# Performance work log

Hardware: AMD Instinct MI355X
Metric: run time of the kernel (lower is better)

Reference implementation:

```python
import jax, jax.numpy as jnp
import numpy as np
from jax import lax

FEAT_STRIDE = 16
RATIOS = (0.5, 1.0, 2.0)
SCALES = (8.0, 16.0, 32.0)
N_ANCHOR = len(RATIOS) * len(SCALES)  # 9
PRE_NMS = 6000     # ProposalCreator test-mode n_pre_nms
POST_NMS = 300     # test-mode n_post_nms
NMS_THRESH = 0.7
MIN_SIZE = 16.0


def _anchor_base():
    base = 16.0
    py = px = base / 2.0
    r = np.asarray(RATIOS, np.float64)
    s = np.asarray(SCALES, np.float64)
    h = (base * s[None, :] * np.sqrt(r[:, None])).reshape(-1)
    w = (base * s[None, :] * np.sqrt(1.0 / r[:, None])).reshape(-1)
    return np.stack([py - h / 2, px - w / 2, py + h / 2, px + w / 2], axis=1).astype(np.float32)  # [9,4] (y1,x1,y2,x2)


def _enumerate_anchors(H, W):
    base = _anchor_base()
    sy = np.arange(H, dtype=np.float32) * FEAT_STRIDE
    sx = np.arange(W, dtype=np.float32) * FEAT_STRIDE
    yy, xx = np.meshgrid(sy, sx, indexing='ij')
    shift = np.stack([yy, xx, yy, xx], axis=-1).reshape(-1, 1, 4)  # [H*W,1,4]
    return jnp.asarray((shift + base[None]).reshape(-1, 4))  # [H*W*9, 4]


def _loc2bbox(anchors, loc):
    h = anchors[:, 2] - anchors[:, 0]
    w = anchors[:, 3] - anchors[:, 1]
    cy = anchors[:, 0] + 0.5 * h
    cx = anchors[:, 1] + 0.5 * w
    dy, dx, dh, dw = loc[:, 0], loc[:, 1], loc[:, 2], loc[:, 3]
    ny, nx = dy * h + cy, dx * w + cx
    nh, nw = jnp.exp(dh) * h, jnp.exp(dw) * w
    return jnp.stack([ny - 0.5 * nh, nx - 0.5 * nw, ny + 0.5 * nh, nx + 0.5 * nw], axis=1)


def _iou_one(box, boxes):
    ty1 = jnp.maximum(box[0], boxes[:, 0])
    tx1 = jnp.maximum(box[1], boxes[:, 1])
    ty2 = jnp.minimum(box[2], boxes[:, 2])
    tx2 = jnp.minimum(box[3], boxes[:, 3])
    inter = jnp.clip(ty2 - ty1, 0.0) * jnp.clip(tx2 - tx1, 0.0)
    a1 = (box[2] - box[0]) * (box[3] - box[1])
    a2 = (boxes[:, 2] - boxes[:, 0]) * (boxes[:, 3] - boxes[:, 1])
    return inter / jnp.maximum(a1 + a2 - inter, 1e-9)


def _nms_keep(boxes, valid):
    # boxes are sorted by descending score; greedy suppression, fixed shapes
    n = boxes.shape[0]
    idxs = jnp.arange(n)
    def body(i, keep):
        iou = _iou_one(boxes[i], boxes)
        sup = (iou > NMS_THRESH) & (idxs > i)
        return jnp.where(keep[i], keep & ~sup, keep)
    return lax.fori_loop(0, n, body, valid)


def _propose_one(loc, fg, anchors, img_h, img_w, scale):
    boxes = _loc2bbox(anchors, loc)
    boxes = jnp.stack([jnp.clip(boxes[:, 0], 0.0, img_h), jnp.clip(boxes[:, 1], 0.0, img_w),
                       jnp.clip(boxes[:, 2], 0.0, img_h), jnp.clip(boxes[:, 3], 0.0, img_w)], axis=1)
    min_sz = MIN_SIZE * scale
    hs = boxes[:, 2] - boxes[:, 0]
    ws = boxes[:, 3] - boxes[:, 1]
    ok = (hs >= min_sz) & (ws >= min_sz)
    sc = jnp.where(ok, fg, -jnp.inf)
    top_sc, top_idx = lax.top_k(sc, PRE_NMS)
    b = boxes[top_idx]
    keep = _nms_keep(b, jnp.isfinite(top_sc))
    # stable-compact kept boxes to the front, pad to POST_NMS with zeros
    order = jnp.argsort(jnp.where(keep, jnp.arange(PRE_NMS), PRE_NMS))
    sel = order[:POST_NMS]
    n_keep = jnp.sum(keep)
    mask = (jnp.arange(POST_NMS) < n_keep)[:, None].astype(b.dtype)
    return b[sel] * mask  # [POST_NMS, 4], zero-padded


def setup_inputs() -> dict:
    key = jax.random.key(0)
    ks = jax.random.split(key, 5)
    B, C, H, W = 16, 512, 50, 50
    x = jax.random.normal(ks[0], (B, C, H, W), jnp.float32)
    conv1_w = 0.01 * jax.random.normal(ks[1], (512, 512, 3, 3), jnp.float32)
    conv1_b = jnp.zeros((512,), jnp.float32)
    score_w = 0.01 * jax.random.normal(ks[2], (N_ANCHOR * 2, 512, 1, 1), jnp.float32)
    score_b = jnp.zeros((N_ANCHOR * 2,), jnp.float32)
    loc_w = 0.01 * jax.random.normal(ks[3], (N_ANCHOR * 4, 512, 1, 1), jnp.float32)
    loc_b = jnp.zeros((N_ANCHOR * 4,), jnp.float32)
    return {"x": x, "img_h": 800, "img_w": 800,
            "conv1_w": conv1_w, "conv1_b": conv1_b,
            "score_w": score_w, "score_b": score_b,
            "loc_w": loc_w, "loc_b": loc_b}


def reference(x, img_h, img_w, conv1_w, conv1_b, score_w, score_b, loc_w, loc_b):
    B, C, H, W = x.shape
    anchors = _enumerate_anchors(H, W)
    # Faithful to the source bug: `mid = self.conv1(x); mid = relu(x)` -> conv1 output is discarded.
    mid = jax.nn.relu(x)
    # 1x1 convs as einsum; permute(0,2,3,1) + view == bhwo layout then reshape
    locs = jnp.einsum('bchw,oc->bhwo', mid, loc_w[:, :, 0, 0]) + loc_b      # [B,H,W,4A]
    locs = locs.reshape(B, -1, 4)                                            # [B, H*W*A, 4]
    scores_raw = jnp.einsum('bchw,oc->bhwo', mid, score_w[:, :, 0, 0]) + score_b  # [B,H,W,2A]
    sm = jax.nn.softmax(scores_raw.reshape(B, H, W, N_ANCHOR, 2), axis=4)
    fg = sm[..., 1].reshape(B, -1)                                           # [B, H*W*A]
    scores = scores_raw.reshape(B, -1, 2)
    ih = jnp.float32(img_h)
    iw = jnp.float32(img_w)
    rois_b = jax.vmap(lambda l, f: _propose_one(l, f, anchors, ih, iw, 1.0))(locs, fg)  # [B,POST,4]
    rois = rois_b.reshape(-1, 4)
    roi_ix = jnp.repeat(jnp.arange(B, dtype=jnp.int32), POST_NMS)
    return locs, scores, rois, roi_ix, anchors
```

## Files before the change

kernel.cpp:

```cpp
#include <hip/hip_runtime.h>
#include <math.h>

#define NB 16
#define PP 2500
#define WWD 50
#define NANCH 22500
#define CIN 512
#define PRE 6000
#define POST 300
#define NW64 94
#define NW32 188
#define NSEG 16
#define SEG 1408
#define SEGP 2048
#define RUN 6016
#define NMST 512

#define OFF_LOCS   0
#define OFF_SCORES 1440000
#define OFF_ROIS   2160000
#define OFF_ROIIX  2179200
#define OFF_ANCH   2184000

typedef unsigned long long u64;
typedef unsigned u32;

__device__ __forceinline__ void g2l16(const float* g, float* l) {
    __builtin_amdgcn_global_load_lds(
        (const __attribute__((address_space(1))) void*)g,
        (__attribute__((address_space(3))) void*)l, 16, 0, 0);
}

__device__ inline float4 anchor_of(int r) {
    int p = r / 9, a = r - p * 9;
    int gy = p / WWD, gx = p - gy * WWD;
    int ri = a / 3, si = a - ri * 3;
    double ratio = (ri == 0) ? 0.5 : (ri == 1 ? 1.0 : 2.0);
    double scale = (si == 0) ? 8.0 : (si == 1 ? 16.0 : 32.0);
    double hh = 16.0 * scale * sqrt(ratio);
    double wd = 16.0 * scale * sqrt(1.0 / ratio);
    float by1 = (float)(8.0 - hh * 0.5);
    float bx1 = (float)(8.0 - wd * 0.5);
    float by2 = (float)(8.0 + hh * 0.5);
    float bx2 = (float)(8.0 + wd * 0.5);
    float sy = (float)gy * 16.0f, sx = (float)gx * 16.0f;
    return make_float4(sy + by1, sx + bx1, sy + by2, sx + bx2);
}

__device__ inline float4 decode_box(const float* __restrict__ lp, float4 an,
                                    float ih, float iw, bool* ok) {
    float dy = lp[0], dx = lp[1], dh = lp[2], dw = lp[3];
    float h = an.z - an.x, w = an.w - an.y;
    float cy = an.x + 0.5f * h, cx = an.y + 0.5f * w;
    float ny = dy * h + cy, nx = dx * w + cx;
    float nh = expf(dh) * h, nw = expf(dw) * w;
    float y1 = fminf(fmaxf(ny - 0.5f * nh, 0.f), ih);
    float x1 = fminf(fmaxf(nx - 0.5f * nw, 0.f), iw);
    float y2 = fminf(fmaxf(ny + 0.5f * nh, 0.f), ih);
    float x2 = fminf(fmaxf(nx + 0.5f * nw, 0.f), iw);
    *ok = ((y2 - y1) >= 16.0f) && ((x2 - x1) >= 16.0f);
    return make_float4(y1, x1, y2, x2);
}

__device__ inline float iou_f32(float4 a, float4 b) {
    float ty1 = fmaxf(a.x, b.x), tx1 = fmaxf(a.y, b.y);
    float ty2 = fminf(a.z, b.z), tx2 = fminf(a.w, b.w);
    float inter = fmaxf(ty2 - ty1, 0.f) * fmaxf(tx2 - tx1, 0.f);
    float aa = (a.z - a.x) * (a.w - a.y);
    float ab = (b.z - b.x) * (b.w - b.y);
    return inter / fmaxf(aa + ab - inter, 1e-9f);
}

__global__ __launch_bounds__(256) void k_gemm(
    const float* __restrict__ x, const float* __restrict__ lw, const float* __restrict__ lb,
    const float* __restrict__ sw, const float* __restrict__ sb, float* __restrict__ out)
{
    __shared__ __align__(16) float wsL[2][64][16];
    __shared__ __align__(16) float xsL[2][16][64];
    int bid = blockIdx.x;
    int b   = bid / 40;
    int pt  = bid % 40;
    int tid = threadIdx.x;
    int po  = tid & 63;
    int wv  = tid >> 6;
    int og  = __builtin_amdgcn_readfirstlane(wv);
    int ptbase = pt * 64;
    int p0  = ptbase + po;
    bool act0 = (p0 < PP);

    int o0  = og * 14;
    int cnt = (og == 3) ? 12 : 14;
    float bias[14];
#pragma unroll
    for (int k = 0; k < 14; ++k) {
        int o = o0 + k;
        int oc = (o < 54) ? o : 53;
        bias[k] = (oc < 36) ? lb[oc] : sb[oc - 36];
    }

    const float* xrow = x + (size_t)b * (CIN * PP);

    float acc0[14];
#pragma unroll
    for (int k = 0; k < 14; ++k) acc0[k] = 0.f;

    auto stage_async = [&](int buf, int c0) {
        {
            int fbase = og * 256 + po * 4;
            int cc = fbase >> 6;
            int xj = fbase & 63;
            int gpos = ptbase + xj;
            if (gpos > PP - 4) gpos = PP - 4;
            const float* gsrc = xrow + (size_t)(c0 + cc) * PP + gpos;
            float* ldst = &xsL[buf][0][0] + og * 256;
            g2l16(gsrc, ldst);
        }
        {
            int fl = og * 256 + po * 4;
            int o = fl >> 4;
            int c4 = fl & 15;
            const float* gw = (o < 36) ? (lw + (size_t)o * CIN + c0 + c4)
                            : (o < 54) ? (sw + (size_t)(o - 36) * CIN + c0 + c4)
                                       : (lw + c4);
            float* wdst = &wsL[buf][0][0] + og * 256;
            g2l16(gw, wdst);
        }
    };

    stage_async(0, 0);
    __syncthreads();

#pragma unroll 1
    for (int t = 0; t < 32; ++t) {
        int cur = t & 1;
        if (t + 1 < 32) stage_async(cur ^ 1, (t + 1) * 16);
#pragma unroll
        for (int g = 0; g < 4; ++g) {
            float x0[4];
#pragma unroll
            for (int u = 0; u < 4; ++u)
                x0[u] = fmaxf(xsL[cur][g * 4 + u][po], 0.f);
#pragma unroll
            for (int k = 0; k < 14; ++k) {
                float4 w4 = *reinterpret_cast<const float4*>(&wsL[cur][o0 + k][g * 4]);
                acc0[k] += x0[0] * w4.x;
                acc0[k] += x0[1] * w4.y;
                acc0[k] += x0[2] * w4.z;
                acc0[k] += x0[3] * w4.w;
            }
        }
        __syncthreads();
    }

    if (!act0) return;
#pragma unroll
    for (int k = 0; k < 14; ++k) {
        if (k < cnt) {
            int o = o0 + k;
            if (o < 36)
                out[(size_t)OFF_LOCS + ((size_t)b * PP + p0) * 36 + o] = acc0[k] + bias[k];
            else
                out[(size_t)OFF_SCORES + ((size_t)b * PP + p0) * 18 + (o - 36)] = acc0[k] + bias[k];
        }
    }
}

__global__ __launch_bounds__(1024) void k_sort1(
    const float* __restrict__ out_ro, float* __restrict__ out, u64* __restrict__ runs,
    const int* __restrict__ imh_p, const int* __restrict__ imw_p)
{
    __shared__ u64 sk[SEGP];
    int blk = blockIdx.x;
    int b = blk >> 4, s = blk & 15;
    int tid = threadIdx.x;
    int base = s * SEG;
    float ih = (float)imh_p[0], iw = (float)imw_p[0];

    for (int i = tid; i < SEGP; i += 1024) {
        int r = base + i;
        u64 key = 0ull;
        if (i < SEG && r < NANCH) {
            float4 an = anchor_of(r);
            if (b == 0) ((float4*)(out + OFF_ANCH))[r] = an;
            bool ok;
            (void)decode_box(out_ro + (size_t)OFF_LOCS + ((size_t)b * NANCH + r) * 4,
                             an, ih, iw, &ok);
            int p = r / 9, a = r - p * 9;
            const float* sp = out_ro + (size_t)OFF_SCORES + ((size_t)b * PP + p) * 18 + a * 2;
            float s0 = sp[0], s1 = sp[1];
            float mx = fmaxf(s0, s1);
            float e0 = expf(s0 - mx), e1 = expf(s1 - mx);
            float fg = e1 / (e0 + e1);
            float sc = ok ? fg : -INFINITY;
            u32 sb = __float_as_uint(sc);
            sb = (sb & 0x80000000u) ? ~sb : (sb | 0x80000000u);
            key = ((u64)sb << 32) | (u64)(u32)(NANCH - r);
        }
        sk[i] = key;
    }
    __syncthreads();
    for (int kk = 2; kk <= SEGP; kk <<= 1) {
        for (int j = kk >> 1; j > 0; j >>= 1) {
            for (int i = tid; i < SEGP; i += 1024) {
                int ij = i ^ j;
                if (ij > i) {
                    u64 va = sk[i], vb = sk[ij];
                    bool up = ((i & kk) == 0);
                    if (up ? (va < vb) : (va > vb)) { sk[i] = vb; sk[ij] = va; }
                }
            }
            __syncthreads();
        }
    }
    u64* dst = runs + (size_t)blk * SEGP;
    for (int i = tid; i < SEGP; i += 1024) dst[i] = sk[i];
}

__device__ inline int mp_search(const u64* A, const u64* B, int LA, int LB, int d) {
    int lo = max(0, d - LB), hi = min(d, LA);
    while (lo < hi) {
        int mid = (lo + hi) >> 1;
        if (A[mid] > B[d - 1 - mid]) lo = mid + 1; else hi = mid;
    }
    return lo;
}

__device__ inline void mp_merge_seg(const u64* A, const u64* B, int LA, int LB,
                                    int d0, int cnt, u64* dst) {
    int i = mp_search(A, B, LA, LB, d0);
    int j = d0 - i;
    for (int e = 0; e < cnt; ++e) {
        u64 va = (i < LA) ? A[i] : 0ull;
        u64 vb = (j < LB) ? B[j] : 0ull;
        bool takeA = (j >= LB) || ((i < LA) && (va > vb));
        dst[d0 + e] = takeA ? va : vb;
        if (takeA) ++i; else ++j;
    }
}

__global__ __launch_bounds__(1024) void k_mergeA(
    const u64* __restrict__ in, u64* __restrict__ outk)
{
    __shared__ u64 bufA[4096];
    __shared__ u64 bufB[4096];
    int blk = blockIdx.x;
    int b = blk >> 2, m = blk & 3;
    int tid = threadIdx.x;
    const u64* s0 = in + ((size_t)b * NSEG + 4 * m) * SEGP;
    const u64* s1 = s0 + SEGP;
    const u64* s2 = s1 + SEGP;
    const u64* s3 = s2 + SEGP;
    mp_merge_seg(s0, s1, SEGP, SEGP, tid * 4, 4, bufA);
    mp_merge_seg(s2, s3, SEGP, SEGP, tid * 4, 4, bufB);
    __syncthreads();
    int d0 = tid * 6;
    if (d0 < RUN)
        mp_merge_seg(bufA, bufB, 4096, 4096, d0, min(6, RUN - d0),
                     outk + ((size_t)b * 4 + m) * RUN);
}

__global__ __launch_bounds__(1024) void k_mergeB_emit(
    const u64* __restrict__ in, const float* __restrict__ out_ro,
    float* __restrict__ topBoxes, u32* __restrict__ topValid,
    const int* __restrict__ imh_p, const int* __restrict__ imw_p)
{
    __shared__ u64 bufA[RUN];
    __shared__ u64 bufB[RUN];
    int b = blockIdx.x;
    int tid = threadIdx.x;
    const u64* r0 = in + (size_t)b * 4 * RUN;
    const u64* r1 = r0 + RUN;
    const u64* r2 = r1 + RUN;
    const u64* r3 = r2 + RUN;
    int d0 = tid * 6;
    if (d0 < RUN) {
        int c = min(6, RUN - d0);
        mp_merge_seg(r0, r1, RUN, RUN, d0, c, bufA);
        mp_merge_seg(r2, r3, RUN, RUN, d0, c, bufB);
    }
    __syncthreads();
    float ih = (float)imh_p[0], iw = (float)imw_p[0];
    if (d0 >= PRE) return;
    int cnt = min(6, PRE - d0);
    int i = mp_search(bufA, bufB, RUN, RUN, d0);
    int j = d0 - i;
    for (int e = 0; e < cnt; ++e) {
        u64 va = (i < RUN) ? bufA[i] : 0ull;
        u64 vb = (j < RUN) ? bufB[j] : 0ull;
        bool takeA = (j >= RUN) || ((i < RUN) && (va > vb));
        u64 key = takeA ? va : vb;
        if (takeA) ++i; else ++j;
        int d = d0 + e;
        bool valid = (key >> 63) != 0ull;
        int idx = valid ? (NANCH - (int)(key & 0xFFFFFFFFull)) : 0;
        bool ok;
        float4 an = anchor_of(idx);
        float4 bx = decode_box(out_ro + (size_t)OFF_LOCS + ((size_t)b * NANCH + idx) * 4,
                               an, ih, iw, &ok);
        ((float4*)topBoxes)[(size_t)b * PRE + d] = bx;
        topValid[(size_t)b * PRE + d] = valid ? 1u : 0u;
    }
}

__global__ __launch_bounds__(NMST) void k_nms(const float* __restrict__ topBoxes,
                                              const u32* __restrict__ topValid,
                                              float* __restrict__ out)
{
    __shared__ float4 chunkB[64];
    __shared__ float4 keptB[POST];
    __shared__ u32 sup[NW32];
    __shared__ int s_nk;
    __shared__ int s_stop;
    int b = blockIdx.x, tid = threadIdx.x;
    int wave = tid >> 6, lane = tid & 63;
    const float4* tb = (const float4*)topBoxes + (size_t)b * PRE;

    for (int i = tid; i < NW32; i += NMST) sup[i] = 0u;
    if (tid == 0) { s_nk = 0; s_stop = 0; }
    __syncthreads();
    for (int r = tid; r < PRE; r += NMST)
        if (!topValid[(size_t)b * PRE + r]) atomicOr(&sup[r >> 5], 1u << (r & 31));
    if (tid == 0) atomicOr(&sup[187], 0xFFFF0000u);
    __syncthreads();

    for (int c = 0; c < NW64; ++c) {
        int base = c * 64;
        if (tid < 64)
            chunkB[tid] = (base + tid < PRE) ? tb[base + tid]
                                             : make_float4(0.f, 0.f, 0.f, 0.f);
        int nk0 = s_nk;
        bool s = false;
        if (nk0 > 0 && base + lane < PRE) {
            float4 bj = tb[base + lane];
            for (int t = wave; t < nk0; t += 8)
                s |= iou_f32(keptB[t], bj) > 0.7f;
        }
        u64 bal = __ballot(s);
        if (lane == 0 && bal) {
            atomicOr(&sup[2 * c], (u32)bal);
            atomicOr(&sup[2 * c + 1], (u32)(bal >> 32));
        }
        __syncthreads();
        if (wave == 0) {
            u64 avail = ~(((u64)sup[2 * c + 1] << 32) | (u64)sup[2 * c]);
            float4 myB = chunkB[lane];
            int nkl = s_nk;
            while (avail && nkl < POST) {
                int i = __builtin_ctzll(avail);
                float4 bi = chunkB[i];
                if (lane == 0) keptB[nkl] = bi;
                nkl++;
                bool ss = iou_f32(bi, myB) > 0.7f;
                u64 bb = __ballot(ss);
                avail &= ~((1ull << i) | bb);
            }
            if (lane == 0) { s_nk = nkl; if (nkl >= POST) s_stop = 1; }
        }
        __syncthreads();
        if (s_stop) break;
    }

    __syncthreads();
    int nk = min(s_nk, POST);
    for (int r = tid; r < POST; r += NMST) {
        float4 v = make_float4(0.f, 0.f, 0.f, 0.f);
        if (r < nk) v = keptB[r];
        ((float4*)(out + OFF_ROIS))[(size_t)b * POST + r] = v;
        out[(size_t)OFF_ROIIX + (size_t)b * POST + r] = (float)b;
    }
}

extern "C" void kernel_launch(void* const* d_in, const int* in_sizes, int n_in,
                              void* d_out, int out_size, void* d_ws, size_t ws_size,
                              hipStream_t stream) {
    const float* x  = (const float*)d_in[0];
    const int* imh  = (const int*)d_in[1];
    const int* imw  = (const int*)d_in[2];
    const float* sw = (const float*)d_in[5];
    const float* sb = (const float*)d_in[6];
    const float* lw = (const float*)d_in[7];
    const float* lb = (const float*)d_in[8];
    float* out = (float*)d_out;
    char* wsb = (char*)d_ws;

    u64*   runs0    = (u64*)(wsb);
    u64*   runs1    = (u64*)(wsb + 4194304);
    float* topBoxes = (float*)(wsb + 7274496);
    u32*   topValid = (u32*)(wsb + 8810496);

    hipLaunchKernelGGL(k_gemm, dim3(NB * 40), dim3(256), 0, stream,
                       x, lw, lb, sw, sb, out);
    hipLaunchKernelGGL(k_sort1, dim3(NB * NSEG), dim3(1024), 0, stream,
                       out, out, runs0, imh, imw);
    hipLaunchKernelGGL(k_mergeA, dim3(NB * 4), dim3(1024), 0, stream,
                       runs0, runs1);
    hipLaunchKernelGGL(k_mergeB_emit, dim3(NB), dim3(1024), 0, stream,
                       runs1, out, topBoxes, topValid, imh, imw);
    hipLaunchKernelGGL(k_nms, dim3(NB), dim3(NMST), 0, stream,
                       topBoxes, topValid, out);
}
```

Before: 232.7 us.

## Stage merge inputs in LDS, split final merge into extra kernel, shrink sort blocks

```diff
diff --git a/kernel.cpp b/kernel.cpp
--- a/kernel.cpp
+++ b/kernel.cpp
@@ -165,7 +165,7 @@
     }
 }
 
-__global__ __launch_bounds__(1024) void k_sort1(
+__global__ __launch_bounds__(256) void k_sort1(
     const float* __restrict__ out_ro, float* __restrict__ out, u64* __restrict__ runs,
     const int* __restrict__ imh_p, const int* __restrict__ imw_p)
 {
@@ -176,7 +176,7 @@
     int base = s * SEG;
     float ih = (float)imh_p[0], iw = (float)imw_p[0];
 
-    for (int i = tid; i < SEGP; i += 1024) {
+    for (int i = tid; i < SEGP; i += 256) {
         int r = base + i;
         u64 key = 0ull;
         if (i < SEG && r < NANCH) {
@@ -201,7 +201,7 @@
     __syncthreads();
     for (int kk = 2; kk <= SEGP; kk <<= 1) {
         for (int j = kk >> 1; j > 0; j >>= 1) {
-            for (int i = tid; i < SEGP; i += 1024) {
+            for (int i = tid; i < SEGP; i += 256) {
                 int ij = i ^ j;
                 if (ij > i) {
                     u64 va = sk[i], vb = sk[ij];
@@ -213,7 +213,7 @@
         }
     }
     u64* dst = runs + (size_t)blk * SEGP;
-    for (int i = tid; i < SEGP; i += 1024) dst[i] = sk[i];
+    for (int i = tid; i < SEGP; i += 256) dst[i] = sk[i];
 }
 
 __device__ inline int mp_search(const u64* A, const u64* B, int LA, int LB, int d) {
@@ -241,17 +241,21 @@
 __global__ __launch_bounds__(1024) void k_mergeA(
     const u64* __restrict__ in, u64* __restrict__ outk)
 {
+    __shared__ u64 stage[4][SEGP];
     __shared__ u64 bufA[4096];
     __shared__ u64 bufB[4096];
     int blk = blockIdx.x;
     int b = blk >> 2, m = blk & 3;
     int tid = threadIdx.x;
-    const u64* s0 = in + ((size_t)b * NSEG + 4 * m) * SEGP;
-    const u64* s1 = s0 + SEGP;
-    const u64* s2 = s1 + SEGP;
-    const u64* s3 = s2 + SEGP;
-    mp_merge_seg(s0, s1, SEGP, SEGP, tid * 4, 4, bufA);
-    mp_merge_seg(s2, s3, SEGP, SEGP, tid * 4, 4, bufB);
+    const u64* src = in + ((size_t)b * NSEG + 4 * m) * SEGP;
+#pragma unroll
+    for (int q = 0; q < 8; ++q) {
+        int lin = q * 1024 + tid;
+        stage[lin >> 11][lin & (SEGP - 1)] = src[lin];
+    }
+    __syncthreads();
+    mp_merge_seg(stage[0], stage[1], SEGP, SEGP, tid * 4, 4, bufA);
+    mp_merge_seg(stage[2], stage[3], SEGP, SEGP, tid * 4, 4, bufB);
     __syncthreads();
     int d0 = tid * 6;
     if (d0 < RUN)
@@ -259,34 +263,44 @@
                      outk + ((size_t)b * 4 + m) * RUN);
 }
 
-__global__ __launch_bounds__(1024) void k_mergeB_emit(
+__global__ __launch_bounds__(1024) void k_mergeB(
+    const u64* __restrict__ in, u64* __restrict__ outk)
+{
+    __shared__ u64 stage[2 * RUN];
+    int blk = blockIdx.x;
+    int b = blk >> 1, h = blk & 1;
+    int tid = threadIdx.x;
+    const u64* src = in + ((size_t)b * 4 + 2 * h) * RUN;
+    for (int lin = tid; lin < 2 * RUN; lin += 1024) stage[lin] = src[lin];
+    __syncthreads();
+    int d0 = tid * 6;
+    if (d0 < RUN)
+        mp_merge_seg(stage, stage + RUN, RUN, RUN, d0, min(6, RUN - d0),
+                     outk + ((size_t)b * 2 + h) * RUN);
+}
+
+__global__ __launch_bounds__(1024) void k_mergeC_emit(
     const u64* __restrict__ in, const float* __restrict__ out_ro,
     float* __restrict__ topBoxes, u32* __restrict__ topValid,
     const int* __restrict__ imh_p, const int* __restrict__ imw_p)
 {
-    __shared__ u64 bufA[RUN];
-    __shared__ u64 bufB[RUN];
+    __shared__ u64 stage[2 * RUN];
     int b = blockIdx.x;
     int tid = threadIdx.x;
-    const u64* r0 = in + (size_t)b * 4 * RUN;
-    const u64* r1 = r0 + RUN;
-    const u64* r2 = r1 + RUN;
-    const u64* r3 = r2 + RUN;
+    const u64* src = in + (size_t)b * 2 * RUN;
+    for (int lin = tid; lin < 2 * RUN; lin += 1024) stage[lin] = src[lin];
+    __syncthreads();
+    float ih = (float)imh_p[0], iw = (float)imw_p[0];
     int d0 = tid * 6;
-    if (d0 < RUN) {
-        int c = min(6, RUN - d0);
-        mp_merge_seg(r0, r1, RUN, RUN, d0, c, bufA);
-        mp_merge_seg(r2, r3, RUN, RUN, d0, c, bufB);
-    }
-    __syncthreads();
-    float ih = (float)imh_p[0], iw = (float)imw_p[0];
     if (d0 >= PRE) return;
     int cnt = min(6, PRE - d0);
-    int i = mp_search(bufA, bufB, RUN, RUN, d0);
+    const u64* A = stage;
+    const u64* B = stage + RUN;
+    int i = mp_search(A, B, RUN, RUN, d0);
     int j = d0 - i;
     for (int e = 0; e < cnt; ++e) {
-        u64 va = (i < RUN) ? bufA[i] : 0ull;
-        u64 vb = (j < RUN) ? bufB[j] : 0ull;
+        u64 va = (i < RUN) ? A[i] : 0ull;
+        u64 vb = (j < RUN) ? B[j] : 0ull;
         bool takeA = (j >= RUN) || ((i < RUN) && (va > vb));
         u64 key = takeA ? va : vb;
         if (takeA) ++i; else ++j;
@@ -385,17 +399,20 @@
 
     u64*   runs0    = (u64*)(wsb);
     u64*   runs1    = (u64*)(wsb + 4194304);
-    float* topBoxes = (float*)(wsb + 7274496);
-    u32*   topValid = (u32*)(wsb + 8810496);
+    u64*   runs2    = (u64*)(wsb + 7274496);
+    float* topBoxes = (float*)(wsb + 8814592);
+    u32*   topValid = (u32*)(wsb + 10350592);
 
     hipLaunchKernelGGL(k_gemm, dim3(NB * 40), dim3(256), 0, stream,
                        x, lw, lb, sw, sb, out);
-    hipLaunchKernelGGL(k_sort1, dim3(NB * NSEG), dim3(1024), 0, stream,
+    hipLaunchKernelGGL(k_sort1, dim3(NB * NSEG), dim3(256), 0, stream,
                        out, out, runs0, imh, imw);
     hipLaunchKernelGGL(k_mergeA, dim3(NB * 4), dim3(1024), 0, stream,
                        runs0, runs1);
-    hipLaunchKernelGGL(k_mergeB_emit, dim3(NB), dim3(1024), 0, stream,
-                       runs1, out, topBoxes, topValid, imh, imw);
+    hipLaunchKernelGGL(k_mergeB, dim3(NB * 2), dim3(1024), 0, stream,
+                       runs1, runs2);
+    hipLaunchKernelGGL(k_mergeC_emit, dim3(NB), dim3(1024), 0, stream,
+                       runs2, out, topBoxes, topValid, imh, imw);
     hipLaunchKernelGGL(k_nms, dim3(NB), dim3(NMST), 0, stream,
                        topBoxes, topValid, out);
 }
```

Result: slower. 274.3 us (+17.9%).
